# Optimization experiments

Measured on AMD Instinct MI355X. Metric: run time of the kernel, lower is better.

Reference implementation:

```python
import jax, jax.numpy as jnp
import numpy as np

EPS = 1e-15

def gmm_conv(x, row, col, pseudo, g_w, mu, sigma, root_w, bias):
    # x: [N,Fin], pseudo: [E,D], g_w: [Fin,K*Fout], mu/sigma: [K,D], root_w: [Fin,Fout]
    N = x.shape[0]
    K, D = mu.shape
    Fout = g_w.shape[1] // K
    gx = (x @ g_w).reshape(N, K, Fout)                       # per-node kernel transforms
    diff = pseudo[:, None, :] - mu[None, :, :]               # [E,K,D]
    gauss = jnp.exp(-0.5 * jnp.sum(diff * diff / (EPS + sigma[None] ** 2), axis=-1))  # [E,K]
    msg = jnp.einsum('ek,eko->eo', gauss, gx[row])           # [E,Fout]
    agg = jax.ops.segment_sum(msg, col, num_segments=N)      # scatter-add to targets
    cnt = jax.ops.segment_sum(jnp.ones((msg.shape[0],), x.dtype), col, num_segments=N)
    agg = agg / jnp.maximum(cnt, 1.0)[:, None]               # mean aggregation (GMMConv default)
    return agg + x @ root_w + bias

def setup_inputs() -> dict:
    key = jax.random.key(0)
    ks = jax.random.split(key, 12)
    N, E, F, H, C, K, D = 50000, 800000, 128, 64, 16, 8, 2
    return {
        'x': jax.random.normal(ks[0], (N, F), jnp.float32),
        'edge_index': jax.random.randint(ks[1], (2, E), 0, N, jnp.int64),
        'edge_attr': jax.random.uniform(ks[2], (E, D), jnp.float32),
        'g1_w': jax.random.normal(ks[3], (F, K * H), jnp.float32) * 0.1,
        'mu1': jax.random.normal(ks[4], (K, D), jnp.float32),
        'sigma1': jax.random.uniform(ks[5], (K, D), jnp.float32) + 0.5,
        'root1_w': jax.random.normal(ks[6], (F, H), jnp.float32) * 0.1,
        'bias1': jnp.zeros((H,), jnp.float32),
        'g2_w': jax.random.normal(ks[7], (H, K * C), jnp.float32) * 0.1,
        'mu2': jax.random.normal(ks[8], (K, D), jnp.float32),
        'sigma2': jax.random.uniform(ks[9], (K, D), jnp.float32) + 0.5,
        'root2_w': jax.random.normal(ks[10], (H, C), jnp.float32) * 0.1,
        'bias2': jnp.zeros((C,), jnp.float32),
    }

def reference(x, edge_index, edge_attr, g1_w, mu1, sigma1, root1_w, bias1,
              g2_w, mu2, sigma2, root2_w, bias2):
    row, col = edge_index[0], edge_index[1]
    # dropout p applied in eval mode -> identity
    h = jax.nn.elu(gmm_conv(x, row, col, edge_attr, g1_w, mu1, sigma1, root1_w, bias1))
    out = gmm_conv(h, row, col, edge_attr, g2_w, mu2, sigma2, root2_w, bias2)
    return jax.nn.log_softmax(out, axis=1)
```

## Files before the change

kernel.cpp:

```cpp
#include <hip/hip_runtime.h>
#include <hip/hip_bf16.h>
#include <hip/hip_fp16.h>
#include <math.h>


#define NF 128
#define NH 64
#define NC 16
#define Z1NODES 16
#define Z1CAP 448
#define E2NODES 16
#define E2CAP 320
#define GXST 160

typedef __bf16 v8bf __attribute__((ext_vector_type(8)));
typedef float v4f __attribute__((ext_vector_type(4)));

__device__ inline ushort f2bu(float x) {
  __hip_bfloat16 h = __float2bfloat16(x);
  return *(ushort*)&h;
}
__device__ inline uint packh2(float a, float b) {
  __half ha = __float2half_rn(a), hb = __float2half_rn(b);
  return (uint)(*(ushort*)&ha) | ((uint)(*(ushort*)&hb) << 16);
}
__device__ inline float2 unph2(uint u) {
  ushort a = (ushort)(u & 0xffff), b = (ushort)(u >> 16);
  return make_float2(__half2float(*(__half*)&a), __half2float(*(__half*)&b));
}
__device__ inline v8bf ld_frag(const ushort* p) {
  uint4 u = *(const uint4*)p;
  return __builtin_bit_cast(v8bf, u);
}

__global__ __launch_bounds__(256) void hist_kernel(const int* __restrict__ col,
                                                   int* __restrict__ counts, int E) {
  int e = blockIdx.x * 256 + threadIdx.x;
  if (e < E) atomicAdd(&counts[col[e]], 1);
}

__global__ __launch_bounds__(256) void scan1_kernel(const int* __restrict__ counts,
                                                    int* __restrict__ starts,
                                                    int* __restrict__ bsums) {
  __shared__ int wsum[4];
  const int t = threadIdx.x, lane = t & 63, wv = t >> 6;
  int4 v = ((const int4*)counts)[blockIdx.x * 256 + t];
  int tsum = v.x + v.y + v.z + v.w;
  int inc = tsum;
  #pragma unroll
  for (int off = 1; off < 64; off <<= 1) {
    int u = __shfl_up(inc, off, 64);
    if (lane >= off) inc += u;
  }
  if (lane == 63) wsum[wv] = inc;
  __syncthreads();
  int wpre = 0;
  for (int j = 0; j < wv; ++j) wpre += wsum[j];
  int excl = wpre + inc - tsum;
  int4 o;
  o.x = excl; o.y = o.x + v.x; o.z = o.y + v.y; o.w = o.z + v.z;
  ((int4*)starts)[blockIdx.x * 256 + t] = o;
  if (t == 255) bsums[blockIdx.x] = excl + tsum;
}

__global__ __launch_bounds__(64) void scan2_kernel(const int* __restrict__ bsums,
                                                   int* __restrict__ bofs, int NB) {
  int lane = threadIdx.x;
  int v = (lane < NB) ? bsums[lane] : 0;
  int inc = v;
  #pragma unroll
  for (int off = 1; off < 64; off <<= 1) {
    int u = __shfl_up(inc, off, 64);
    if (lane >= off) inc += u;
  }
  if (lane < NB) bofs[lane] = inc - v;
}

__global__ __launch_bounds__(256) void scan3_kernel(int* __restrict__ starts,
                                                    int* __restrict__ cursor,
                                                    const int* __restrict__ bofs) {
  int add = bofs[blockIdx.x];
  int idx = blockIdx.x * 256 + threadIdx.x;
  int4 s = ((int4*)starts)[idx];
  s.x += add; s.y += add; s.z += add; s.w += add;
  ((int4*)starts)[idx] = s;
  ((int4*)cursor)[idx] = s;
}

__global__ __launch_bounds__(256) void fill_kernel(
    const int* __restrict__ row, const int* __restrict__ col,
    const float* __restrict__ eattr,
    const float* __restrict__ mu1, const float* __restrict__ sg1,
    const float* __restrict__ mu2, const float* __restrict__ sg2,
    int* __restrict__ cursor, int* __restrict__ erow,
    uint4* __restrict__ ew1, uint4* __restrict__ ew2, int E) {
  int e = blockIdx.x * 256 + threadIdx.x;
  if (e >= E) return;
  int c = col[e];
  int pos = atomicAdd(&cursor[c], 1);
  float p0 = eattr[2 * e], p1 = eattr[2 * e + 1];
  float w1[8], w2[8];
  #pragma unroll
  for (int k = 0; k < 8; ++k) {
    float d0 = p0 - mu1[2 * k], d1 = p1 - mu1[2 * k + 1];
    float s0 = sg1[2 * k], s1 = sg1[2 * k + 1];
    w1[k] = __expf(-0.5f * (d0 * d0 / (1e-15f + s0 * s0) +
                            d1 * d1 / (1e-15f + s1 * s1)));
    float e0 = p0 - mu2[2 * k], e1 = p1 - mu2[2 * k + 1];
    float t0 = sg2[2 * k], t1 = sg2[2 * k + 1];
    w2[k] = __expf(-0.5f * (e0 * e0 / (1e-15f + t0 * t0) +
                            e1 * e1 / (1e-15f + t1 * t1)));
  }
  erow[pos] = row[e];
  ew1[pos] = make_uint4(packh2(w1[0], w1[1]), packh2(w1[2], w1[3]),
                        packh2(w1[4], w1[5]), packh2(w1[6], w1[7]));
  ew2[pos] = make_uint4(packh2(w2[0], w2[1]), packh2(w2[2], w2[3]),
                        packh2(w2[4], w2[5]), packh2(w2[6], w2[7]));
}

__global__ __launch_bounds__(256) void cast_x_kernel(const float* __restrict__ x,
                                                     ushort* __restrict__ A1, int N) {
  int idx = blockIdx.x * 256 + threadIdx.x;
  if (idx >= N * 32) return;
  int n = idx >> 5, c4 = idx & 31;
  float4 v = ((const float4*)x)[idx];
  ushort4 o;
  o.x = f2bu(v.x); o.y = f2bu(v.y); o.z = f2bu(v.z); o.w = f2bu(v.w);
  *(ushort4*)(A1 + (size_t)n * 1152 + 1024 + c4 * 4) = o;
}

__global__ __launch_bounds__(256) void prep_kernel(
    const float* __restrict__ g1w, const float* __restrict__ r1w,
    const float* __restrict__ g2w, const float* __restrict__ r2w,
    ushort* __restrict__ W1t, ushort* __restrict__ G2pT) {
  int i = blockIdx.x * 256 + threadIdx.x;
  if (i < 64 * 1152) {
    int h = i / 1152, j = i % 1152;
    float v = (j < 1024) ? g1w[(size_t)(j & 127) * 512 + (j >> 7) * 64 + h]
                         : r1w[(size_t)(j - 1024) * 64 + h];
    W1t[i] = f2bu(v);
  } else {
    int i2 = i - 64 * 1152;
    if (i2 < 144 * 64) {
      int cp = i2 / 64, f = i2 % 64;
      float v;
      if (cp < 128) {
        int kq = cp >> 5, rem = cp & 31;
        int o = rem >> 1, k = kq * 2 + (rem & 1);
        v = g2w[(size_t)f * 128 + k * 16 + o];
      } else {
        v = r2w[(size_t)f * 16 + (cp - 128)];
      }
      G2pT[i2] = f2bu(v);
    }
  }
}

__global__ __launch_bounds__(256) void z1_kernel(
    ushort* __restrict__ A1, const int* __restrict__ erow,
    const uint4* __restrict__ ew1, const int* __restrict__ starts, int N) {
  __shared__ __align__(16) float lw[Z1CAP + 8][8];
  __shared__ int loff[Z1CAP + 8];
  const int t = threadIdx.x, lane = t & 63, wv = t >> 6;
  const int base = (int)blockIdx.x * Z1NODES;
  const int S = starts[base];
  const int cl = min(starts[base + Z1NODES] - S, Z1CAP);
  for (int i = t; i < cl; i += 256) {
    loff[i] = erow[S + i] * 2304;
    uint4 qq = ew1[S + i];
    float2 a = unph2(qq.x), b = unph2(qq.y), c = unph2(qq.z), d = unph2(qq.w);
    *(float4*)&lw[i][0] = make_float4(a.x, a.y, b.x, b.y);
    *(float4*)&lw[i][4] = make_float4(c.x, c.y, d.x, d.y);
  }
  if (t < 8) {
    loff[cl + t] = 0;
    *(float4*)&lw[cl + t][0] = make_float4(0.f, 0.f, 0.f, 0.f);
    *(float4*)&lw[cl + t][4] = make_float4(0.f, 0.f, 0.f, 0.f);
  }
  __syncthreads();

  const char* xb = (const char*)(A1 + 1024) + (lane << 2);

  for (int i = 0; i < Z1NODES / 4; ++i) {
    const int n = base + wv * 4 + i;
    const int be = starts[n], ee = starts[n + 1];
    float a0[8], a1[8];
    #pragma unroll
    for (int k = 0; k < 8; ++k) { a0[k] = 0.f; a1[k] = 0.f; }

    const int reRel = min(ee - S, cl);
    for (int q = min(be - S, cl); q < reRel; q += 8) {
      int off[8];
      #pragma unroll
      for (int u = 0; u < 8; ++u) off[u] = loff[q + u];
      uint g[8];
      #pragma unroll
      for (int u = 0; u < 8; ++u) g[u] = *(const uint*)(xb + off[u]);
      #pragma unroll
      for (int u = 0; u < 8; ++u) {
        const bool ok = (q + u) < reRel;
        float4 wl = *(float4*)&lw[q + u][0];
        float4 wh = *(float4*)&lw[q + u][4];
        float f0 = ok ? __uint_as_float(g[u] << 16) : 0.f;
        float f1 = ok ? __uint_as_float(g[u] & 0xffff0000u) : 0.f;
        a0[0] = fmaf(wl.x, f0, a0[0]); a1[0] = fmaf(wl.x, f1, a1[0]);
        a0[1] = fmaf(wl.y, f0, a0[1]); a1[1] = fmaf(wl.y, f1, a1[1]);
        a0[2] = fmaf(wl.z, f0, a0[2]); a1[2] = fmaf(wl.z, f1, a1[2]);
        a0[3] = fmaf(wl.w, f0, a0[3]); a1[3] = fmaf(wl.w, f1, a1[3]);
        a0[4] = fmaf(wh.x, f0, a0[4]); a1[4] = fmaf(wh.x, f1, a1[4]);
        a0[5] = fmaf(wh.y, f0, a0[5]); a1[5] = fmaf(wh.y, f1, a1[5]);
        a0[6] = fmaf(wh.z, f0, a0[6]); a1[6] = fmaf(wh.z, f1, a1[6]);
        a0[7] = fmaf(wh.w, f0, a0[7]); a1[7] = fmaf(wh.w, f1, a1[7]);
      }
    }
    for (int j = max(S + reRel, be); j < ee; ++j) {
      uint4 qq = ew1[j];
      uint g = *(const uint*)(xb + erow[j] * 2304);
      float2 a = unph2(qq.x), b = unph2(qq.y), c = unph2(qq.z), d = unph2(qq.w);
      float f0 = __uint_as_float(g << 16);
      float f1 = __uint_as_float(g & 0xffff0000u);
      a0[0] = fmaf(a.x, f0, a0[0]); a1[0] = fmaf(a.x, f1, a1[0]);
      a0[1] = fmaf(a.y, f0, a0[1]); a1[1] = fmaf(a.y, f1, a1[1]);
      a0[2] = fmaf(b.x, f0, a0[2]); a1[2] = fmaf(b.x, f1, a1[2]);
      a0[3] = fmaf(b.y, f0, a0[3]); a1[3] = fmaf(b.y, f1, a1[3]);
      a0[4] = fmaf(c.x, f0, a0[4]); a1[4] = fmaf(c.x, f1, a1[4]);
      a0[5] = fmaf(c.y, f0, a0[5]); a1[5] = fmaf(c.y, f1, a1[5]);
      a0[6] = fmaf(d.x, f0, a0[6]); a1[6] = fmaf(d.x, f1, a1[6]);
      a0[7] = fmaf(d.y, f0, a0[7]); a1[7] = fmaf(d.y, f1, a1[7]);
    }
    const float inv = 1.f / fmaxf((float)(ee - be), 1.f);
    ushort* zr = A1 + (size_t)n * 1152;
    #pragma unroll
    for (int k = 0; k < 8; ++k) {
      uint pk = (uint)f2bu(a0[k] * inv) | ((uint)f2bu(a1[k] * inv) << 16);
      *(uint*)(zr + k * 128 + 2 * lane) = pk;
    }
  }
}

__global__ __launch_bounds__(256) void gemm1_mfma(
    const ushort* __restrict__ A1, const ushort* __restrict__ W1t,
    const float* __restrict__ b1, ushort* __restrict__ h_bf, int N) {
  __shared__ __align__(16) ushort As[2][64 * 32];
  __shared__ __align__(16) ushort Bs[2][64 * 32];
  const int t = threadIdx.x, lane = t & 63, wv = t >> 6;
  const int mfrag = lane & 15, quad = lane >> 4;
  const int m0 = (int)blockIdx.x * 64;
  const int st_r = t >> 2, st_c = (t & 3) * 8;
  const int st_o = st_r * 32 + st_c;
  const ushort* ag = A1 + (size_t)(m0 + st_r) * 1152 + st_c;
  const ushort* bg = W1t + (size_t)st_r * 1152 + st_c;

  {
    uint4 a0 = *(const uint4*)ag;
    uint4 b0 = *(const uint4*)bg;
    *(uint4*)(&As[0][st_o]) = a0;
    *(uint4*)(&Bs[0][st_o]) = b0;
  }
  __syncthreads();

  v4f acc[4];
  #pragma unroll
  for (int ct = 0; ct < 4; ++ct) acc[ct] = (v4f){0.f, 0.f, 0.f, 0.f};

  for (int kc = 0; kc < 36; ++kc) {
    const int cb = kc & 1, nb = cb ^ 1;
    uint4 an, bn;
    if (kc < 35) {
      an = *(const uint4*)(ag + (kc + 1) * 32);
      bn = *(const uint4*)(bg + (kc + 1) * 32);
    }
    v8bf a = ld_frag(&As[cb][(wv * 16 + mfrag) * 32 + quad * 8]);
    #pragma unroll
    for (int ct = 0; ct < 4; ++ct) {
      v8bf b = ld_frag(&Bs[cb][(ct * 16 + mfrag) * 32 + quad * 8]);
      acc[ct] = __builtin_amdgcn_mfma_f32_16x16x32_bf16(a, b, acc[ct], 0, 0, 0);
    }
    if (kc < 35) {
      *(uint4*)(&As[nb][st_o]) = an;
      *(uint4*)(&Bs[nb][st_o]) = bn;
      __syncthreads();
    }
  }
  #pragma unroll
  for (int ct = 0; ct < 4; ++ct) {
    const int colh = ct * 16 + mfrag;
    const float bc = b1[colh];
    #pragma unroll
    for (int r = 0; r < 4; ++r) {
      int node = m0 + wv * 16 + quad * 4 + r;
      if (node < N) {
        float v = acc[ct][r] + bc;
        v = v > 0.f ? v : expm1f(v);
        h_bf[(size_t)node * NH + colh] = f2bu(v);
      }
    }
  }
}

__global__ __launch_bounds__(256) void gemm2a_kernel(
    const ushort* __restrict__ h_bf, const ushort* __restrict__ G2pT,
    ushort* __restrict__ gx2e, int N) {
  const int t = threadIdx.x, lane = t & 63, wv = t >> 6;
  const int mfrag = lane & 15, quad = lane >> 4;
  const int m0 = (int)blockIdx.x * 64 + wv * 16;
  v4f acc[9];
  #pragma unroll
  for (int t9 = 0; t9 < 9; ++t9) acc[t9] = (v4f){0.f, 0.f, 0.f, 0.f};
  const ushort* arow = h_bf + (size_t)(m0 + mfrag) * 64 + quad * 8;
  const ushort* brow = G2pT + (size_t)mfrag * 64 + quad * 8;
  #pragma unroll
  for (int kc = 0; kc < 2; ++kc) {
    v8bf a = ld_frag(arow + kc * 32);
    #pragma unroll
    for (int t9 = 0; t9 < 9; ++t9) {
      v8bf b = ld_frag(brow + (size_t)t9 * 16 * 64 + kc * 32);
      acc[t9] = __builtin_amdgcn_mfma_f32_16x16x32_bf16(a, b, acc[t9], 0, 0, 0);
    }
  }
  #pragma unroll
  for (int t9 = 0; t9 < 9; ++t9) {
    #pragma unroll
    for (int r = 0; r < 4; ++r) {
      int node = m0 + quad * 4 + r;
      if (node < N)
        gx2e[(size_t)node * GXST + t9 * 16 + mfrag] = f2bu(acc[t9][r]);
    }
  }
}

__global__ __launch_bounds__(256) void edge2_kernel(
    const ushort* __restrict__ gx2e, const int* __restrict__ erow,
    const uint4* __restrict__ ew2, const int* __restrict__ starts,
    const float* __restrict__ b2, float* __restrict__ out, int N) {
  __shared__ __align__(16) float lw[E2CAP + 8][8];
  __shared__ int loff[E2CAP + 8];
  __shared__ float lb2[16];
  const int t = threadIdx.x, lane = t & 63, wv = t >> 6;
  const int base = (int)blockIdx.x * E2NODES;
  const int S = starts[base];
  const int cl = min(starts[base + E2NODES] - S, E2CAP);
  if (t < 16) lb2[t] = b2[t];
  for (int i = t; i < cl; i += 256) {
    loff[i] = erow[S + i] * 320;
    uint4 qq = ew2[S + i];
    float2 a = unph2(qq.x), b = unph2(qq.y), c = unph2(qq.z), d = unph2(qq.w);
    *(float4*)&lw[i][0] = make_float4(a.x, a.y, b.x, b.y);
    *(float4*)&lw[i][4] = make_float4(c.x, c.y, d.x, d.y);
  }
  if (t < 8) {
    loff[cl + t] = 0;
    *(float4*)&lw[cl + t][0] = make_float4(0.f, 0.f, 0.f, 0.f);
    *(float4*)&lw[cl + t][4] = make_float4(0.f, 0.f, 0.f, 0.f);
  }
  __syncthreads();

  const int o = lane & 15, kq = lane >> 4;
  const char* gb = (const char*)gx2e + kq * 64 + o * 4;

  for (int i = 0; i < E2NODES / 4; ++i) {
    const int n = base + wv * 4 + i;
    if (n >= N) continue;
    const int be = starts[n], ee = starts[n + 1];
    float acc0 = 0.f, acc1 = 0.f;
    const int reRel = min(ee - S, cl);
    for (int q = min(be - S, cl); q < reRel; q += 8) {
      int off[8];
      #pragma unroll
      for (int u = 0; u < 8; ++u) off[u] = loff[q + u];
      uint g[8];
      #pragma unroll
      for (int u = 0; u < 8; ++u) g[u] = *(const uint*)(gb + off[u]);
      #pragma unroll
      for (int u = 0; u < 8; ++u) {
        const bool ok = (q + u) < reRel;
        float2 w = *(float2*)&lw[q + u][kq * 2];
        float f0 = ok ? __uint_as_float(g[u] << 16) : 0.f;
        float f1 = ok ? __uint_as_float(g[u] & 0xffff0000u) : 0.f;
        acc0 = fmaf(w.x, f0, acc0);
        acc1 = fmaf(w.y, f1, acc1);
      }
    }
    for (int j = max(S + reRel, be); j < ee; ++j) {
      uint4 qq = ew2[j];
      uint comp = (kq == 0) ? qq.x : (kq == 1) ? qq.y : (kq == 2) ? qq.z : qq.w;
      float2 wp = unph2(comp);
      uint g = *(const uint*)(gb + erow[j] * 320);
      float f0 = __uint_as_float(g << 16);
      float f1 = __uint_as_float(g & 0xffff0000u);
      acc0 = fmaf(wp.x, f0, acc0);
      acc1 = fmaf(wp.y, f1, acc1);
    }
    float s = acc0 + acc1;
    s += __shfl_xor(s, 16, 64);
    s += __shfl_xor(s, 32, 64);
    const float inv = 1.f / fmaxf((float)(ee - be), 1.f);
    ushort ru = *((const ushort*)gx2e + (size_t)n * GXST + 128 + o);
    float root = __uint_as_float(((uint)ru) << 16);
    float v = s * inv + root + lb2[o];
    float mx = v;
    #pragma unroll
    for (int off = 8; off >= 1; off >>= 1) mx = fmaxf(mx, __shfl_xor(mx, off, 64));
    float sm = __expf(v - mx);
    #pragma unroll
    for (int off = 8; off >= 1; off >>= 1) sm += __shfl_xor(sm, off, 64);
    if (kq == 0) out[(size_t)n * NC + o] = v - mx - __logf(sm);
  }
}

extern "C" void kernel_launch(void* const* d_in, const int* in_sizes, int n_in,
                              void* d_out, int out_size, void* d_ws, size_t ws_size,
                              hipStream_t stream) {
  const float* x     = (const float*)d_in[0];
  const int*   eidx  = (const int*)d_in[1];
  const float* eattr = (const float*)d_in[2];
  const float* g1w   = (const float*)d_in[3];
  const float* mu1   = (const float*)d_in[4];
  const float* sg1   = (const float*)d_in[5];
  const float* r1w   = (const float*)d_in[6];
  const float* b1    = (const float*)d_in[7];
  const float* g2w   = (const float*)d_in[8];
  const float* mu2   = (const float*)d_in[9];
  const float* sg2   = (const float*)d_in[10];
  const float* r2w   = (const float*)d_in[11];
  const float* b2    = (const float*)d_in[12];

  const int N = in_sizes[0] / NF;
  const int E = in_sizes[1] / 2;
  const int* row = eidx;
  const int* col = eidx + E;
  const int N2 = (N + 63) & ~63;
  const int NP = (N + 1023) & ~1023;
  const int NB = NP / 1024;

  uint4* ew1   = (uint4*)d_ws;
  uint4* ew2   = ew1 + (size_t)E;
  ushort* A1   = (ushort*)(ew2 + (size_t)E);
  ushort* gx2e = A1;
  ushort* h_bf = A1 + (size_t)N2 * 1152;
  ushort* W1t  = h_bf + (size_t)N2 * NH;
  ushort* G2pT = W1t + (size_t)64 * 1152;
  int* erow    = (int*)(G2pT + (size_t)144 * 64);
  int* counts  = erow + (size_t)E;
  int* starts  = counts + NP;
  int* cursor  = starts + NP;
  int* bsums   = cursor + NP;
  int* bofs    = bsums + 64;

  hipMemsetAsync(counts, 0, (size_t)NP * sizeof(int), stream);
  hist_kernel<<<(E + 255) / 256, 256, 0, stream>>>(col, counts, E);
  scan1_kernel<<<NB, 256, 0, stream>>>(counts, starts, bsums);
  scan2_kernel<<<1, 64, 0, stream>>>(bsums, bofs, NB);
  scan3_kernel<<<NB, 256, 0, stream>>>(starts, cursor, bofs);
  fill_kernel<<<(E + 255) / 256, 256, 0, stream>>>(row, col, eattr, mu1, sg1,
                                                   mu2, sg2, cursor, erow,
                                                   ew1, ew2, E);
  cast_x_kernel<<<(N * 32 + 255) / 256, 256, 0, stream>>>(x, A1, N);
  prep_kernel<<<(64 * 1152 + 144 * 64 + 255) / 256, 256, 0, stream>>>(
      g1w, r1w, g2w, r2w, W1t, G2pT);

  z1_kernel<<<N / Z1NODES, 256, 0, stream>>>(A1, erow, ew1, starts, N);
  gemm1_mfma<<<N2 / 64, 256, 0, stream>>>(A1, W1t, b1, h_bf, N);
  gemm2a_kernel<<<N2 / 64, 256, 0, stream>>>(h_bf, G2pT, gx2e, N);
  edge2_kernel<<<(N + E2NODES - 1) / E2NODES, 256, 0, stream>>>(
      gx2e, erow, ew2, starts, b2, (float*)d_out, N);
}
```

Before: 329.5 us.

## Compute Gaussian edge weights on the fly from a permuted edge record

```diff
diff --git a/kernel.cpp b/kernel.cpp
--- a/kernel.cpp
+++ b/kernel.cpp
@@ -20,23 +20,22 @@
   __hip_bfloat16 h = __float2bfloat16(x);
   return *(ushort*)&h;
 }
-__device__ inline uint packh2(float a, float b) {
-  __half ha = __float2half_rn(a), hb = __float2half_rn(b);
-  return (uint)(*(ushort*)&ha) | ((uint)(*(ushort*)&hb) << 16);
-}
-__device__ inline float2 unph2(uint u) {
-  ushort a = (ushort)(u & 0xffff), b = (ushort)(u >> 16);
-  return make_float2(__half2float(*(__half*)&a), __half2float(*(__half*)&b));
-}
 __device__ inline v8bf ld_frag(const ushort* p) {
   uint4 u = *(const uint4*)p;
   return __builtin_bit_cast(v8bf, u);
 }
 
-__global__ __launch_bounds__(256) void hist_kernel(const int* __restrict__ col,
-                                                   int* __restrict__ counts, int E) {
+__global__ __launch_bounds__(256) void hist_kernel(
+    const int* __restrict__ col, const int* __restrict__ row,
+    const float* __restrict__ eattr, int* __restrict__ counts,
+    uint4* __restrict__ rec, int E) {
   int e = blockIdx.x * 256 + threadIdx.x;
-  if (e < E) atomicAdd(&counts[col[e]], 1);
+  if (e >= E) return;
+  atomicAdd(&counts[col[e]], 1);
+  int r = row[e];
+  float2 p = *(const float2*)(eattr + 2 * e);
+  rec[e] = make_uint4((uint)(r * 2304), __float_as_uint(p.x),
+                      __float_as_uint(p.y), (uint)(r * 320));
 }
 
 __global__ __launch_bounds__(256) void scan1_kernel(const int* __restrict__ counts,
@@ -87,35 +86,14 @@
   ((int4*)cursor)[idx] = s;
 }
 
-__global__ __launch_bounds__(256) void fill_kernel(
-    const int* __restrict__ row, const int* __restrict__ col,
-    const float* __restrict__ eattr,
-    const float* __restrict__ mu1, const float* __restrict__ sg1,
-    const float* __restrict__ mu2, const float* __restrict__ sg2,
-    int* __restrict__ cursor, int* __restrict__ erow,
-    uint4* __restrict__ ew1, uint4* __restrict__ ew2, int E) {
+__global__ __launch_bounds__(256) void perm_kernel(const int* __restrict__ col,
+                                                   int* __restrict__ cursor,
+                                                   int* __restrict__ perm, int E) {
   int e = blockIdx.x * 256 + threadIdx.x;
-  if (e >= E) return;
-  int c = col[e];
-  int pos = atomicAdd(&cursor[c], 1);
-  float p0 = eattr[2 * e], p1 = eattr[2 * e + 1];
-  float w1[8], w2[8];
-  #pragma unroll
-  for (int k = 0; k < 8; ++k) {
-    float d0 = p0 - mu1[2 * k], d1 = p1 - mu1[2 * k + 1];
-    float s0 = sg1[2 * k], s1 = sg1[2 * k + 1];
-    w1[k] = __expf(-0.5f * (d0 * d0 / (1e-15f + s0 * s0) +
-                            d1 * d1 / (1e-15f + s1 * s1)));
-    float e0 = p0 - mu2[2 * k], e1 = p1 - mu2[2 * k + 1];
-    float t0 = sg2[2 * k], t1 = sg2[2 * k + 1];
-    w2[k] = __expf(-0.5f * (e0 * e0 / (1e-15f + t0 * t0) +
-                            e1 * e1 / (1e-15f + t1 * t1)));
-  }
-  erow[pos] = row[e];
-  ew1[pos] = make_uint4(packh2(w1[0], w1[1]), packh2(w1[2], w1[3]),
-                        packh2(w1[4], w1[5]), packh2(w1[6], w1[7]));
-  ew2[pos] = make_uint4(packh2(w2[0], w2[1]), packh2(w2[2], w2[3]),
-                        packh2(w2[4], w2[5]), packh2(w2[6], w2[7]));
+  if (e < E) {
+    int pos = atomicAdd(&cursor[col[e]], 1);
+    perm[pos] = e;
+  }
 }
 
 __global__ __launch_bounds__(256) void cast_x_kernel(const float* __restrict__ x,
@@ -157,20 +135,37 @@
 }
 
 __global__ __launch_bounds__(256) void z1_kernel(
-    ushort* __restrict__ A1, const int* __restrict__ erow,
-    const uint4* __restrict__ ew1, const int* __restrict__ starts, int N) {
+    ushort* __restrict__ A1, const int* __restrict__ perm,
+    const uint4* __restrict__ rec, const float* __restrict__ mu1,
+    const float* __restrict__ sg1, const int* __restrict__ starts, int N) {
   __shared__ __align__(16) float lw[Z1CAP + 8][8];
   __shared__ int loff[Z1CAP + 8];
   const int t = threadIdx.x, lane = t & 63, wv = t >> 6;
   const int base = (int)blockIdx.x * Z1NODES;
   const int S = starts[base];
   const int cl = min(starts[base + Z1NODES] - S, Z1CAP);
+
+  float mk[16], ck[16];
+  #pragma unroll
+  for (int k = 0; k < 16; ++k) {
+    float s = sg1[k];
+    mk[k] = -0.5f / (1e-15f + s * s);
+    ck[k] = mu1[k];
+  }
+
   for (int i = t; i < cl; i += 256) {
-    loff[i] = erow[S + i] * 2304;
-    uint4 qq = ew1[S + i];
-    float2 a = unph2(qq.x), b = unph2(qq.y), c = unph2(qq.z), d = unph2(qq.w);
-    *(float4*)&lw[i][0] = make_float4(a.x, a.y, b.x, b.y);
-    *(float4*)&lw[i][4] = make_float4(c.x, c.y, d.x, d.y);
+    int e = perm[S + i];
+    uint4 r = rec[e];
+    loff[i] = (int)r.x;
+    float p0 = __uint_as_float(r.y), p1 = __uint_as_float(r.z);
+    float w[8];
+    #pragma unroll
+    for (int k = 0; k < 8; ++k) {
+      float d0 = p0 - ck[2 * k], d1 = p1 - ck[2 * k + 1];
+      w[k] = __expf(fmaf(d0 * d0, mk[2 * k], d1 * d1 * mk[2 * k + 1]));
+    }
+    *(float4*)&lw[i][0] = make_float4(w[0], w[1], w[2], w[3]);
+    *(float4*)&lw[i][4] = make_float4(w[4], w[5], w[6], w[7]);
   }
   if (t < 8) {
     loff[cl + t] = 0;
@@ -214,19 +209,19 @@
       }
     }
     for (int j = max(S + reRel, be); j < ee; ++j) {
-      uint4 qq = ew1[j];
-      uint g = *(const uint*)(xb + erow[j] * 2304);
-      float2 a = unph2(qq.x), b = unph2(qq.y), c = unph2(qq.z), d = unph2(qq.w);
+      int e = perm[j];
+      uint4 r = rec[e];
+      uint g = *(const uint*)(xb + (int)r.x);
+      float p0 = __uint_as_float(r.y), p1 = __uint_as_float(r.z);
       float f0 = __uint_as_float(g << 16);
       float f1 = __uint_as_float(g & 0xffff0000u);
-      a0[0] = fmaf(a.x, f0, a0[0]); a1[0] = fmaf(a.x, f1, a1[0]);
-      a0[1] = fmaf(a.y, f0, a0[1]); a1[1] = fmaf(a.y, f1, a1[1]);
-      a0[2] = fmaf(b.x, f0, a0[2]); a1[2] = fmaf(b.x, f1, a1[2]);
-      a0[3] = fmaf(b.y, f0, a0[3]); a1[3] = fmaf(b.y, f1, a1[3]);
-      a0[4] = fmaf(c.x, f0, a0[4]); a1[4] = fmaf(c.x, f1, a1[4]);
-      a0[5] = fmaf(c.y, f0, a0[5]); a1[5] = fmaf(c.y, f1, a1[5]);
-      a0[6] = fmaf(d.x, f0, a0[6]); a1[6] = fmaf(d.x, f1, a1[6]);
-      a0[7] = fmaf(d.y, f0, a0[7]); a1[7] = fmaf(d.y, f1, a1[7]);
+      #pragma unroll
+      for (int k = 0; k < 8; ++k) {
+        float d0 = p0 - ck[2 * k], d1 = p1 - ck[2 * k + 1];
+        float w = __expf(fmaf(d0 * d0, mk[2 * k], d1 * d1 * mk[2 * k + 1]));
+        a0[k] = fmaf(w, f0, a0[k]);
+        a1[k] = fmaf(w, f1, a1[k]);
+      }
     }
     const float inv = 1.f / fmaxf((float)(ee - be), 1.f);
     ushort* zr = A1 + (size_t)n * 1152;
@@ -330,8 +325,9 @@
 }
 
 __global__ __launch_bounds__(256) void edge2_kernel(
-    const ushort* __restrict__ gx2e, const int* __restrict__ erow,
-    const uint4* __restrict__ ew2, const int* __restrict__ starts,
+    const ushort* __restrict__ gx2e, const int* __restrict__ perm,
+    const uint4* __restrict__ rec, const float* __restrict__ mu2,
+    const float* __restrict__ sg2, const int* __restrict__ starts,
     const float* __restrict__ b2, float* __restrict__ out, int N) {
   __shared__ __align__(16) float lw[E2CAP + 8][8];
   __shared__ int loff[E2CAP + 8];
@@ -341,12 +337,28 @@
   const int S = starts[base];
   const int cl = min(starts[base + E2NODES] - S, E2CAP);
   if (t < 16) lb2[t] = b2[t];
+
+  float mk[16], ck[16];
+  #pragma unroll
+  for (int k = 0; k < 16; ++k) {
+    float s = sg2[k];
+    mk[k] = -0.5f / (1e-15f + s * s);
+    ck[k] = mu2[k];
+  }
+
   for (int i = t; i < cl; i += 256) {
-    loff[i] = erow[S + i] * 320;
-    uint4 qq = ew2[S + i];
-    float2 a = unph2(qq.x), b = unph2(qq.y), c = unph2(qq.z), d = unph2(qq.w);
-    *(float4*)&lw[i][0] = make_float4(a.x, a.y, b.x, b.y);
-    *(float4*)&lw[i][4] = make_float4(c.x, c.y, d.x, d.y);
+    int e = perm[S + i];
+    uint4 r = rec[e];
+    loff[i] = (int)r.w;
+    float p0 = __uint_as_float(r.y), p1 = __uint_as_float(r.z);
+    float w[8];
+    #pragma unroll
+    for (int k = 0; k < 8; ++k) {
+      float d0 = p0 - ck[2 * k], d1 = p1 - ck[2 * k + 1];
+      w[k] = __expf(fmaf(d0 * d0, mk[2 * k], d1 * d1 * mk[2 * k + 1]));
+    }
+    *(float4*)&lw[i][0] = make_float4(w[0], w[1], w[2], w[3]);
+    *(float4*)&lw[i][4] = make_float4(w[4], w[5], w[6], w[7]);
   }
   if (t < 8) {
     loff[cl + t] = 0;
@@ -357,6 +369,10 @@
 
   const int o = lane & 15, kq = lane >> 4;
   const char* gb = (const char*)gx2e + kq * 64 + o * 4;
+  const float tu0 = mu2[2 * kq], tu1 = mu2[2 * kq + 1];
+  const float ts0 = sg2[2 * kq], ts1 = sg2[2 * kq + 1];
+  const float tm0 = -0.5f / (1e-15f + ts0 * ts0);
+  const float tm1 = -0.5f / (1e-15f + ts1 * ts1);
 
   for (int i = 0; i < E2NODES / 4; ++i) {
     const int n = base + wv * 4 + i;
@@ -382,14 +398,31 @@
       }
     }
     for (int j = max(S + reRel, be); j < ee; ++j) {
-      uint4 qq = ew2[j];
-      uint comp = (kq == 0) ? qq.x : (kq == 1) ? qq.y : (kq == 2) ? qq.z : qq.w;
-      float2 wp = unph2(comp);
-      uint g = *(const uint*)(gb + erow[j] * 320);
+      int e = perm[j];
+      uint4 r = rec[e];
+      uint g = *(const uint*)(gb + (int)r.w);
+      float p0 = __uint_as_float(r.y), p1 = __uint_as_float(r.z);
+      float d0 = p0 - tu0, d1 = p1 - tu1;
+      float w0 = __expf(d0 * d0 * tm0 + d1 * d1 * tm1);
       float f0 = __uint_as_float(g << 16);
       float f1 = __uint_as_float(g & 0xffff0000u);
-      acc0 = fmaf(wp.x, f0, acc0);
-      acc1 = fmaf(wp.y, f1, acc1);
+      acc0 = fmaf(w0, f0, acc0);
+      {
+        float e0 = p0 - tu1;
+        (void)e0;
+      }
+      float du0 = p0 - tu1;
+      (void)du0;
+      acc1 = fmaf(__expf((p0 - tu1) * (p0 - tu1) * 0.f +
+                         0.f), 0.f, acc1) * 1.f;
+      acc1 = acc1;
+      float q0 = p0 - mu2[2 * (2 * kq + 1)];
+      float q1 = p1 - mu2[2 * (2 * kq + 1) + 1];
+      float ss0 = sg2[2 * (2 * kq + 1)];
+      float ss1 = sg2[2 * (2 * kq + 1) + 1];
+      float w1v = __expf(-0.5f * (q0 * q0 / (1e-15f + ss0 * ss0) +
+                                  q1 * q1 / (1e-15f + ss1 * ss1)));
+      acc1 = fmaf(w1v, f1, acc1);
     }
     float s = acc0 + acc1;
     s += __shfl_xor(s, 16, 64);
@@ -433,35 +466,32 @@
   const int NP = (N + 1023) & ~1023;
   const int NB = NP / 1024;
 
-  uint4* ew1   = (uint4*)d_ws;
-  uint4* ew2   = ew1 + (size_t)E;
-  ushort* A1   = (ushort*)(ew2 + (size_t)E);
+  uint4* rec   = (uint4*)d_ws;
+  ushort* A1   = (ushort*)(rec + (size_t)E);
   ushort* gx2e = A1;
   ushort* h_bf = A1 + (size_t)N2 * 1152;
   ushort* W1t  = h_bf + (size_t)N2 * NH;
   ushort* G2pT = W1t + (size_t)64 * 1152;
-  int* erow    = (int*)(G2pT + (size_t)144 * 64);
-  int* counts  = erow + (size_t)E;
+  int* perm    = (int*)(G2pT + (size_t)144 * 64);
+  int* counts  = perm + (size_t)E;
   int* starts  = counts + NP;
   int* cursor  = starts + NP;
   int* bsums   = cursor + NP;
   int* bofs    = bsums + 64;
 
   hipMemsetAsync(counts, 0, (size_t)NP * sizeof(int), stream);
-  hist_kernel<<<(E + 255) / 256, 256, 0, stream>>>(col, counts, E);
+  hist_kernel<<<(E + 255) / 256, 256, 0, stream>>>(col, row, eattr, counts, rec, E);
   scan1_kernel<<<NB, 256, 0, stream>>>(counts, starts, bsums);
   scan2_kernel<<<1, 64, 0, stream>>>(bsums, bofs, NB);
   scan3_kernel<<<NB, 256, 0, stream>>>(starts, cursor, bofs);
-  fill_kernel<<<(E + 255) / 256, 256, 0, stream>>>(row, col, eattr, mu1, sg1,
-                                                   mu2, sg2, cursor, erow,
-                                                   ew1, ew2, E);
+  perm_kernel<<<(E + 255) / 256, 256, 0, stream>>>(col, cursor, perm, E);
   cast_x_kernel<<<(N * 32 + 255) / 256, 256, 0, stream>>>(x, A1, N);
   prep_kernel<<<(64 * 1152 + 144 * 64 + 255) / 256, 256, 0, stream>>>(
       g1w, r1w, g2w, r2w, W1t, G2pT);
 
-  z1_kernel<<<N / Z1NODES, 256, 0, stream>>>(A1, erow, ew1, starts, N);
+  z1_kernel<<<N / Z1NODES, 256, 0, stream>>>(A1, perm, rec, mu1, sg1, starts, N);
   gemm1_mfma<<<N2 / 64, 256, 0, stream>>>(A1, W1t, b1, h_bf, N);
   gemm2a_kernel<<<N2 / 64, 256, 0, stream>>>(h_bf, G2pT, gx2e, N);
   edge2_kernel<<<(N + E2NODES - 1) / E2NODES, 256, 0, stream>>>(
-      gx2e, erow, ew2, starts, b2, (float*)d_out, N);
-}
+      gx2e, perm, rec, mu2, sg2, starts, b2, (float*)d_out, N);
+}
```

Result: slower. 352.6 us (+7.0%).
